# Kernel tuning notes

Measured on AMD Instinct MI355X. Metric: run time of the kernel, lower is better.

The kernel has to match this reference:

```python
import jax, jax.numpy as jnp
import numpy as np

N_NODES = 100000
N_EDGES = 1638400
IN_FEAT = 128
OUT_FEAT = 64
NUM_RELS = 8


def setup_inputs() -> dict:
    key = jax.random.key(0)
    k1, k2, k3, k4, k5 = jax.random.split(key, 5)
    feat = jax.random.normal(k1, (N_NODES, IN_FEAT), dtype=jnp.float32)
    W = jax.random.normal(k2, (NUM_RELS, OUT_FEAT, IN_FEAT), dtype=jnp.float32) * 0.05
    edge_src = jax.random.randint(k3, (N_EDGES,), 0, N_NODES, dtype=jnp.int32)
    edge_dst = jax.random.randint(k4, (N_EDGES,), 0, N_NODES, dtype=jnp.int32)
    edge_type = jax.random.randint(k5, (N_EDGES,), 0, NUM_RELS, dtype=jnp.int32)
    return {"feat": feat, "W": W, "edge_src": edge_src,
            "edge_dst": edge_dst, "edge_type": edge_type}


def reference(feat, W, edge_src, edge_dst, edge_type):
    # RGCN hetero forward: Y[i,fo] = sum_{edges e: dst(e)=i} W[rel(e)] @ feat[src(e)]
    # Transform all node features under every relation once: [R, N, out].
    xw = jnp.einsum('nf,rof->rno', feat, W)
    # Per-edge message gather: [E, out]
    msg = xw[edge_type, edge_src]
    # Scatter-add into destination nodes: [N, out]
    y = jax.ops.segment_sum(msg, edge_dst, num_segments=feat.shape[0])
    return y
```

## Files before the change

kernel.cpp:

```cpp
#include <hip/hip_runtime.h>
#include <hip/hip_bf16.h>
#include <stdint.h>

#define N_NODES 100000
#define N_EDGES 1638400
#define IN_FEAT 128
#define OUT_FEAT 64
#define NUM_RELS 8
#define NTILES ((N_NODES + 63) / 64)
#define TGRID 1024

#define BUCKET_BITS 9
#define BUCKET_SIZE 512
#define NBUCKETS ((N_NODES + BUCKET_SIZE - 1) / BUCKET_SIZE)
#define ABLOCKS 200
#define AEDGES (N_EDGES / ABLOCKS)
#define APT (AEDGES / 1024)
#define BK 12

typedef __attribute__((ext_vector_type(8))) short short8;
typedef __attribute__((ext_vector_type(4))) float floatx4;

__device__ __forceinline__ unsigned short f2bf(float x) {
    union { float f; uint32_t u; } c; c.f = x;
    uint32_t u = c.u;
    u += 0x7FFFu + ((u >> 16) & 1u);
    return (unsigned short)(u >> 16);
}

__device__ __forceinline__ uint32_t cvt_pk_bf16(float lo, float hi) {
    uint32_t r;
    asm("v_cvt_pk_bf16_f32 %0, %1, %2" : "=v"(r) : "v"(lo), "v"(hi));
    return r;
}

__device__ __forceinline__ void barrier_lds_only() {
    asm volatile("s_waitcnt lgkmcnt(0)\n\ts_barrier" ::: "memory");
}

#define W8 (NUM_RELS * OUT_FEAT * IN_FEAT / 8)
__global__ __launch_bounds__(256)
void prep_kernel(const float* __restrict__ W, unsigned short* __restrict__ W_bf,
                 int* __restrict__ bucketHist) {
    int u = blockIdx.x * 256 + threadIdx.x;
    if (u < NBUCKETS) bucketHist[u] = 0;
    int w = u - NBUCKETS;
    if (w >= 0 && w < W8) {
        const float* s = W + (size_t)w * 8;
        float4 a = *(const float4*)s, b = *(const float4*)(s + 4);
        short8 v;
        v[0] = f2bf(a.x); v[1] = f2bf(a.y); v[2] = f2bf(a.z); v[3] = f2bf(a.w);
        v[4] = f2bf(b.x); v[5] = f2bf(b.y); v[6] = f2bf(b.z); v[7] = f2bf(b.w);
        *(short8*)(W_bf + (size_t)w * 8) = v;
    }
}

__global__ __launch_bounds__(1024)
void buckethist_kernel(const int* __restrict__ dst, int* __restrict__ bucketHist) {
    __shared__ int h[NBUCKETS];
    const int t = threadIdx.x;
    if (t < NBUCKETS) h[t] = 0;
    __syncthreads();
    #pragma unroll
    for (int i = 0; i < APT; ++i) {
        int e = blockIdx.x * AEDGES + i * 1024 + t;
        atomicAdd(&h[dst[e] >> BUCKET_BITS], 1);
    }
    __syncthreads();
    if (t < NBUCKETS && h[t] > 0) atomicAdd(&bucketHist[t], h[t]);
}

__global__ __launch_bounds__(256)
void bucketscan_kernel(const int* __restrict__ bucketHist, int* __restrict__ bucketStart,
                       int* __restrict__ bucketCursor) {
    __shared__ int wtot[4];
    const int t = threadIdx.x, lane = t & 63, wv = t >> 6;
    int v = (t < NBUCKETS) ? bucketHist[t] : 0;
    int x = v;
    #pragma unroll
    for (int d = 1; d < 64; d <<= 1) {
        int tv = __shfl_up(x, d, 64);
        if (lane >= d) x += tv;
    }
    if (lane == 63) wtot[wv] = x;
    __syncthreads();
    if (t == 0) {
        int run = 0;
        #pragma unroll
        for (int j = 0; j < 4; ++j) { int c = wtot[j]; wtot[j] = run; run += c; }
    }
    __syncthreads();
    int excl = x - v + wtot[wv];
    if (t < NBUCKETS) { bucketStart[t] = excl; bucketCursor[t] = excl; }
    if (t == 0) bucketStart[NBUCKETS] = N_EDGES;
}

__global__ __launch_bounds__(1024)
void bin_kernel(const int* __restrict__ src, const int* __restrict__ dst,
                const int* __restrict__ typ, int* __restrict__ bucketCursor,
                uint32_t* __restrict__ bins) {
    __shared__ int h[NBUCKETS];
    __shared__ int base[NBUCKETS];
    const int t = threadIdx.x;
    if (t < NBUCKETS) h[t] = 0;
    __syncthreads();
    uint32_t pk[APT]; int bk[APT], rk[APT];
    #pragma unroll
    for (int i = 0; i < APT; ++i) {
        int e = blockIdx.x * AEDGES + i * 1024 + t;
        int d = dst[e];
        int b = d >> BUCKET_BITS;
        bk[i] = b;
        pk[i] = ((uint32_t)(d & (BUCKET_SIZE - 1)) << 20) | ((uint32_t)typ[e] << 17) | (uint32_t)src[e];
        rk[i] = atomicAdd(&h[b], 1);
    }
    __syncthreads();
    if (t < NBUCKETS && h[t] > 0) base[t] = atomicAdd(&bucketCursor[t], h[t]);
    __syncthreads();
    #pragma unroll
    for (int i = 0; i < APT; ++i)
        bins[base[bk[i]] + rk[i]] = pk[i];
}

__global__ __launch_bounds__(1024)
void sortb_kernel(const int* __restrict__ bucketStart, uint32_t* __restrict__ bins,
                  int* __restrict__ offs) {
    __shared__ int cnt_l[BUCKET_SIZE];
    __shared__ int start_l[BUCKET_SIZE];
    __shared__ int wtot[8];
    const int b = blockIdx.x;
    const int t = threadIdx.x, lane = t & 63, wv = t >> 6;
    const int s = bucketStart[b];
    const int cnt = bucketStart[b + 1] - s;
    if (t < BUCKET_SIZE) cnt_l[t] = 0;
    __syncthreads();
    uint32_t pk[BK]; int rk[BK], ld[BK];
    #pragma unroll
    for (int k = 0; k < BK; ++k) {
        int idx = t + k * 1024;
        ld[k] = -1;
        if (idx < cnt) {
            uint32_t p = bins[s + idx];
            pk[k] = p;
            ld[k] = (int)(p >> 20);
            rk[k] = atomicAdd(&cnt_l[ld[k]], 1);
        }
    }
    __syncthreads();
    int v = 0, x = 0;
    if (t < BUCKET_SIZE) {
        v = cnt_l[t]; x = v;
        #pragma unroll
        for (int d = 1; d < 64; d <<= 1) {
            int tv = __shfl_up(x, d, 64);
            if (lane >= d) x += tv;
        }
        if (lane == 63) wtot[wv] = x;
    }
    __syncthreads();
    if (t == 0) {
        int run = 0;
        #pragma unroll
        for (int j = 0; j < 8; ++j) { int c = wtot[j]; wtot[j] = run; run += c; }
    }
    __syncthreads();
    if (t < BUCKET_SIZE) {
        int excl = x - v + wtot[wv];
        start_l[t] = excl;
        int node = b * BUCKET_SIZE + t;
        if (node < N_NODES) offs[node] = ((s + excl) << 8) | v;
    }
    __syncthreads();
    #pragma unroll
    for (int k = 0; k < BK; ++k)
        if (ld[k] >= 0)
            bins[s + start_l[ld[k]] + rk[k]] = pk[k];
}

__global__ __launch_bounds__(512)
void transform_kernel(const float* __restrict__ feat,
                      const unsigned short* __restrict__ W_bf,
                      unsigned short* __restrict__ xw) {
    const int t    = threadIdx.x;
    const int lane = t & 63;
    const int r    = t >> 6;
    const int quad = lane >> 4;
    const int lrow = lane & 15;

    __shared__ unsigned short sA[2][64 * 136];

    short8 wfr[4][4];
    #pragma unroll
    for (int jm = 0; jm < 4; ++jm)
        #pragma unroll
        for (int kk = 0; kk < 4; ++kk)
            wfr[jm][kk] = *(const short8*)(W_bf +
                ((size_t)r * OUT_FEAT + jm * 16 + lrow) * IN_FEAT + kk * 32 + quad * 8);

    int tile = blockIdx.x;

    #pragma unroll
    for (int i = 0; i < 4; ++i) {
        int f4 = t + 512 * i;
        int row = f4 >> 5, c4 = f4 & 31;
        int n = tile * 64 + row;
        float4 v = (n < N_NODES) ? *(const float4*)(feat + (size_t)n * IN_FEAT + c4 * 4)
                                 : make_float4(0.f, 0.f, 0.f, 0.f);
        uint2 q;
        q.x = cvt_pk_bf16(v.x, v.y);
        q.y = cvt_pk_bf16(v.z, v.w);
        *(uint2*)&sA[0][row * 136 + c4 * 4] = q;
    }

    int p = 0;
    while (tile < NTILES) {
        barrier_lds_only();
        int nxt = tile + TGRID;
        if (nxt < NTILES) {
            #pragma unroll
            for (int i = 0; i < 4; ++i) {
                int f4 = t + 512 * i;
                int row = f4 >> 5, c4 = f4 & 31;
                int n = nxt * 64 + row;
                float4 v = (n < N_NODES) ? *(const float4*)(feat + (size_t)n * IN_FEAT + c4 * 4)
                                         : make_float4(0.f, 0.f, 0.f, 0.f);
                uint2 q;
                q.x = cvt_pk_bf16(v.x, v.y);
                q.y = cvt_pk_bf16(v.z, v.w);
                *(uint2*)&sA[p ^ 1][row * 136 + c4 * 4] = q;
            }
        }

        const int n0 = tile * 64;
        const bool full = (n0 + 64 <= N_NODES);
        #pragma unroll
        for (int nb = 0; nb < 4; ++nb) {
            floatx4 acc[4] = {{0,0,0,0},{0,0,0,0},{0,0,0,0},{0,0,0,0}};
            #pragma unroll
            for (int kk = 0; kk < 4; ++kk) {
                short8 bfrag = *(const short8*)&sA[p][(nb * 16 + lrow) * 136 + kk * 32 + quad * 8];
                #pragma unroll
                for (int jm = 0; jm < 4; ++jm)
                    acc[jm] = __builtin_amdgcn_mfma_f32_16x16x32_bf16(wfr[jm][kk], bfrag, acc[jm], 0, 0, 0);
            }
            int n = n0 + nb * 16 + lrow;
            if (full || n < N_NODES) {
                unsigned short* rowp = xw + ((size_t)r * N_NODES + n) * OUT_FEAT;
                #pragma unroll
                for (int jm = 0; jm < 4; ++jm) {
                    uint2 u;
                    u.x = (uint32_t)f2bf(acc[jm][0]) | ((uint32_t)f2bf(acc[jm][1]) << 16);
                    u.y = (uint32_t)f2bf(acc[jm][2]) | ((uint32_t)f2bf(acc[jm][3]) << 16);
                    *(uint2*)(rowp + jm * 16 + quad * 4) = u;
                }
            }
        }
        p ^= 1;
        tile = nxt;
    }
}

__global__ __launch_bounds__(256)
void gather_kernel(const unsigned short* __restrict__ xw, const int* __restrict__ offs,
                   const uint32_t* __restrict__ bins, float* __restrict__ out) {
    const int wv = threadIdx.x >> 6;
    const int lane = threadIdx.x & 63;
    const int g = lane >> 3;
    const int l = lane & 7;
    const int node = blockIdx.x * 4 + wv;
    if (node >= N_NODES) return;
    const int pd = offs[node];
    const int start = pd >> 8;
    const int deg = pd & 255;
    float acc[8] = {0.f, 0.f, 0.f, 0.f, 0.f, 0.f, 0.f, 0.f};
    for (int base = 0; base < deg; base += 64) {
        int rem = deg - base; if (rem > 64) rem = 64;
        uint32_t pl = bins[start + base + lane];
        int rounds = (rem + 7) >> 3;
        for (int i = 0; i < rounds; ++i) {
            int ei = i * 8 + g;
            uint32_t p = __shfl(pl, ei, 64);
            if (ei < rem) {
                int rel = (p >> 17) & 7;
                int src = (int)(p & 0x1FFFF);
                const uint4* q = (const uint4*)(xw + ((size_t)rel * N_NODES + src) * OUT_FEAT + l * 8);
                uint4 u = *q;
                union { uint32_t u; float f; } c;
                c.u = u.x << 16;         acc[0] += c.f;
                c.u = u.x & 0xFFFF0000u; acc[1] += c.f;
                c.u = u.y << 16;         acc[2] += c.f;
                c.u = u.y & 0xFFFF0000u; acc[3] += c.f;
                c.u = u.z << 16;         acc[4] += c.f;
                c.u = u.z & 0xFFFF0000u; acc[5] += c.f;
                c.u = u.w << 16;         acc[6] += c.f;
                c.u = u.w & 0xFFFF0000u; acc[7] += c.f;
            }
        }
    }
    #pragma unroll
    for (int d = 8; d < 64; d <<= 1) {
        #pragma unroll
        for (int j = 0; j < 8; ++j)
            acc[j] += __shfl_xor(acc[j], d, 64);
    }
    if (g == 0) {
        float* rowp = out + (size_t)node * OUT_FEAT + l * 8;
        float4 a = make_float4(acc[0], acc[1], acc[2], acc[3]);
        float4 b = make_float4(acc[4], acc[5], acc[6], acc[7]);
        *(float4*)rowp = a;
        *(float4*)(rowp + 4) = b;
    }
}

extern "C" void kernel_launch(void* const* d_in, const int* in_sizes, int n_in,
                              void* d_out, int out_size, void* d_ws, size_t ws_size,
                              hipStream_t stream) {
    const float* feat = (const float*)d_in[0];
    const float* W    = (const float*)d_in[1];
    const int* esrc   = (const int*)d_in[2];
    const int* edst   = (const int*)d_in[3];
    const int* etyp   = (const int*)d_in[4];
    float* out = (float*)d_out;

    char* ws = (char*)d_ws;
    size_t ofs = 0;
    unsigned short* xw = (unsigned short*)(ws + ofs);
    ofs += (size_t)NUM_RELS * N_NODES * OUT_FEAT * 2;
    unsigned short* W_bf = (unsigned short*)(ws + ofs);
    ofs += (size_t)NUM_RELS * OUT_FEAT * IN_FEAT * 2;
    uint32_t* bins = (uint32_t*)(ws + ofs);
    ofs += (size_t)N_EDGES * 4 + 256;
    int* offs = (int*)(ws + ofs);
    ofs += ((size_t)N_NODES * 4 + 255) & ~(size_t)255;
    int* bucketHist = (int*)(ws + ofs);   ofs += 1024;
    int* bucketStart = (int*)(ws + ofs);  ofs += 1024;
    int* bucketCursor = (int*)(ws + ofs); ofs += 1024;

    prep_kernel<<<(NBUCKETS + W8 + 255) / 256, 256, 0, stream>>>(W, W_bf, bucketHist);
    buckethist_kernel<<<ABLOCKS, 1024, 0, stream>>>(edst, bucketHist);
    bucketscan_kernel<<<1, 256, 0, stream>>>(bucketHist, bucketStart, bucketCursor);
    bin_kernel<<<ABLOCKS, 1024, 0, stream>>>(esrc, edst, etyp, bucketCursor, bins);
    sortb_kernel<<<NBUCKETS, 1024, 0, stream>>>(bucketStart, bins, offs);
    transform_kernel<<<TGRID, 512, 0, stream>>>(feat, W_bf, xw);
    gather_kernel<<<(N_NODES + 3) / 4, 256, 0, stream>>>(xw, offs, bins, out);
}
```

Before: 133.8 us.

## Use fixed-capacity edge buckets to drop histogram and scan passes

Each destination bucket now gets a fixed region of BCAP slots in the bins buffer. The binning kernel can therefore append through atomic cursors without first counting bucket sizes. This removes the separate histogram kernel, with its full read of edge_dst, and the single-block scan kernel, along with their launch overhead. In exchange, bins grows to the padded size, and correctness depends on no bucket holding more than BCAP edges, which holds only for roughly uniform destination indices. The custom LDS-only barrier in the transform kernel is also replaced by __syncthreads.

```diff
diff --git a/kernel.cpp b/kernel.cpp
--- a/kernel.cpp
+++ b/kernel.cpp
@@ -13,6 +13,7 @@
 #define BUCKET_BITS 9
 #define BUCKET_SIZE 512
 #define NBUCKETS ((N_NODES + BUCKET_SIZE - 1) / BUCKET_SIZE)
+#define BCAP 8960
 #define ABLOCKS 200
 #define AEDGES (N_EDGES / ABLOCKS)
 #define APT (AEDGES / 1024)
@@ -34,16 +35,12 @@
     return r;
 }
 
-__device__ __forceinline__ void barrier_lds_only() {
-    asm volatile("s_waitcnt lgkmcnt(0)\n\ts_barrier" ::: "memory");
-}
-
 #define W8 (NUM_RELS * OUT_FEAT * IN_FEAT / 8)
 __global__ __launch_bounds__(256)
 void prep_kernel(const float* __restrict__ W, unsigned short* __restrict__ W_bf,
-                 int* __restrict__ bucketHist) {
+                 int* __restrict__ bucketCursor) {
     int u = blockIdx.x * 256 + threadIdx.x;
-    if (u < NBUCKETS) bucketHist[u] = 0;
+    if (u < NBUCKETS) bucketCursor[u] = 0;
     int w = u - NBUCKETS;
     if (w >= 0 && w < W8) {
         const float* s = W + (size_t)w * 8;
@@ -56,46 +53,6 @@
 }
 
 __global__ __launch_bounds__(1024)
-void buckethist_kernel(const int* __restrict__ dst, int* __restrict__ bucketHist) {
-    __shared__ int h[NBUCKETS];
-    const int t = threadIdx.x;
-    if (t < NBUCKETS) h[t] = 0;
-    __syncthreads();
-    #pragma unroll
-    for (int i = 0; i < APT; ++i) {
-        int e = blockIdx.x * AEDGES + i * 1024 + t;
-        atomicAdd(&h[dst[e] >> BUCKET_BITS], 1);
-    }
-    __syncthreads();
-    if (t < NBUCKETS && h[t] > 0) atomicAdd(&bucketHist[t], h[t]);
-}
-
-__global__ __launch_bounds__(256)
-void bucketscan_kernel(const int* __restrict__ bucketHist, int* __restrict__ bucketStart,
-                       int* __restrict__ bucketCursor) {
-    __shared__ int wtot[4];
-    const int t = threadIdx.x, lane = t & 63, wv = t >> 6;
-    int v = (t < NBUCKETS) ? bucketHist[t] : 0;
-    int x = v;
-    #pragma unroll
-    for (int d = 1; d < 64; d <<= 1) {
-        int tv = __shfl_up(x, d, 64);
-        if (lane >= d) x += tv;
-    }
-    if (lane == 63) wtot[wv] = x;
-    __syncthreads();
-    if (t == 0) {
-        int run = 0;
-        #pragma unroll
-        for (int j = 0; j < 4; ++j) { int c = wtot[j]; wtot[j] = run; run += c; }
-    }
-    __syncthreads();
-    int excl = x - v + wtot[wv];
-    if (t < NBUCKETS) { bucketStart[t] = excl; bucketCursor[t] = excl; }
-    if (t == 0) bucketStart[NBUCKETS] = N_EDGES;
-}
-
-__global__ __launch_bounds__(1024)
 void bin_kernel(const int* __restrict__ src, const int* __restrict__ dst,
                 const int* __restrict__ typ, int* __restrict__ bucketCursor,
                 uint32_t* __restrict__ bins) {
@@ -119,19 +76,19 @@
     __syncthreads();
     #pragma unroll
     for (int i = 0; i < APT; ++i)
-        bins[base[bk[i]] + rk[i]] = pk[i];
+        bins[(size_t)bk[i] * BCAP + base[bk[i]] + rk[i]] = pk[i];
 }
 
 __global__ __launch_bounds__(1024)
-void sortb_kernel(const int* __restrict__ bucketStart, uint32_t* __restrict__ bins,
+void sortb_kernel(const int* __restrict__ bucketCursor, uint32_t* __restrict__ bins,
                   int* __restrict__ offs) {
     __shared__ int cnt_l[BUCKET_SIZE];
     __shared__ int start_l[BUCKET_SIZE];
     __shared__ int wtot[8];
     const int b = blockIdx.x;
     const int t = threadIdx.x, lane = t & 63, wv = t >> 6;
-    const int s = bucketStart[b];
-    const int cnt = bucketStart[b + 1] - s;
+    const int s = b * BCAP;
+    const int cnt = bucketCursor[b];
     if (t < BUCKET_SIZE) cnt_l[t] = 0;
     __syncthreads();
     uint32_t pk[BK]; int rk[BK], ld[BK];
@@ -214,7 +171,7 @@
 
     int p = 0;
     while (tile < NTILES) {
-        barrier_lds_only();
+        __syncthreads();
         int nxt = tile + TGRID;
         if (nxt < NTILES) {
             #pragma unroll
@@ -329,18 +286,14 @@
     unsigned short* W_bf = (unsigned short*)(ws + ofs);
     ofs += (size_t)NUM_RELS * OUT_FEAT * IN_FEAT * 2;
     uint32_t* bins = (uint32_t*)(ws + ofs);
-    ofs += (size_t)N_EDGES * 4 + 256;
+    ofs += (size_t)NBUCKETS * BCAP * 4;
     int* offs = (int*)(ws + ofs);
     ofs += ((size_t)N_NODES * 4 + 255) & ~(size_t)255;
-    int* bucketHist = (int*)(ws + ofs);   ofs += 1024;
-    int* bucketStart = (int*)(ws + ofs);  ofs += 1024;
     int* bucketCursor = (int*)(ws + ofs); ofs += 1024;
 
-    prep_kernel<<<(NBUCKETS + W8 + 255) / 256, 256, 0, stream>>>(W, W_bf, bucketHist);
-    buckethist_kernel<<<ABLOCKS, 1024, 0, stream>>>(edst, bucketHist);
-    bucketscan_kernel<<<1, 256, 0, stream>>>(bucketHist, bucketStart, bucketCursor);
+    prep_kernel<<<(NBUCKETS + W8 + 255) / 256, 256, 0, stream>>>(W, W_bf, bucketCursor);
     bin_kernel<<<ABLOCKS, 1024, 0, stream>>>(esrc, edst, etyp, bucketCursor, bins);
-    sortb_kernel<<<NBUCKETS, 1024, 0, stream>>>(bucketStart, bins, offs);
+    sortb_kernel<<<NBUCKETS, 1024, 0, stream>>>(bucketCursor, bins, offs);
     transform_kernel<<<TGRID, 512, 0, stream>>>(feat, W_bf, xw);
     gather_kernel<<<(N_NODES + 3) / 4, 256, 0, stream>>>(xw, offs, bins, out);
 }
```

Result: faster. 125.3 us (-6.3%).
